# Kernel optimization log

Measured on AMD Instinct MI355X. Metric: run time of the kernel, lower is better.

The kernel has to match this reference:

```python
import jax, jax.numpy as jnp
import numpy as np

N_ATT, N_HEAD, D_K, D_IN = 4, 8, 64, 512
B, T = 128, 512
TEMP = float(np.sqrt(D_K))  # temperature = d_k ** 0.5


def setup_inputs() -> dict:
    key = jax.random.key(0)
    k1, k2, k3 = jax.random.split(key, 3)
    v = jax.random.normal(k1, (B, T, D_IN), jnp.float32)
    # nn.Parameter Q init: normal(0, sqrt(2/d_k))
    Q = jax.random.normal(k2, (N_ATT, N_HEAD, D_K), jnp.float32) * np.sqrt(2.0 / D_K)
    # fc1_k: Linear(d_in, num_attention*n_head*d_k), weight ~ N(0, sqrt(2/d_k))
    Wk = jax.random.normal(k3, (N_ATT * N_HEAD * D_K, D_IN), jnp.float32) * np.sqrt(2.0 / D_K)
    bk = jnp.zeros((N_ATT * N_HEAD * D_K,), jnp.float32)
    return {"v": v, "Q": Q, "Wk": Wk, "bk": bk}


def reference(v, Q, Wk, bk):
    A, H, dk = Q.shape
    Bsz, Tt, d_in = v.shape
    c = d_in // H  # per-head value channels

    # q = stack(Q, dim=2 over batch).view(-1, d_k)  -> [A*H*B, d_k]
    q = jnp.broadcast_to(Q[:, :, None, :], (A, H, Bsz, dk)).reshape(-1, dk)

    # k = fc1_k(v).view(B,T,A,H,dk).permute(3,0,1,2,4).contiguous().view(-1,T,dk)
    # NOTE: this view is a raw C-order reinterpretation (scrambles t/A axes);
    # transpose + reshape reproduces torch's contiguous().view() exactly.
    k = (v @ Wk.T + bk).reshape(Bsz, Tt, A, H, dk)
    k = jnp.transpose(k, (3, 0, 1, 2, 4)).reshape(-1, Tt, dk)  # [H*B*A, T, dk]

    # v heads: stack(v.split(c, dim=-1)).view(H*B, T, c)
    vh = jnp.transpose(v.reshape(Bsz, Tt, H, c), (2, 0, 1, 3)).reshape(H * Bsz, Tt, c)

    # single-query scaled dot-product attention (dropout in eval mode -> identity)
    attn = jnp.einsum('xd,xtd->xt', q, k) / TEMP  # [A*H*B, T]
    attn = jax.nn.softmax(attn, axis=-1)

    # v[:, None].expand(-1, A, -1, -1).reshape(-1, T, c)
    vexp = jnp.broadcast_to(vh[:, None], (H * Bsz, A, Tt, c)).reshape(-1, Tt, c)
    out = jnp.einsum('xt,xtc->xc', attn, vexp)  # [A*H*B, c]

    output = out.reshape(A, H, Bsz, c)
    attn = attn.reshape(A, H, Bsz, Tt)
    return output, attn
```

## Files before the change

kernel.cpp:

```cpp
#include <hip/hip_runtime.h>
#include <hip/hip_bf16.h>
#include <math.h>

#define DIN 512
#define TT  512
#define BSZ 128

using bf16x8 = __attribute__((ext_vector_type(8))) short;
using f32x4  = __attribute__((ext_vector_type(4))) float;

static __device__ __forceinline__ unsigned short f2bf(float x) {
    __hip_bfloat16 h = __float2bfloat16(x);
    return *reinterpret_cast<unsigned short*>(&h);
}
static __device__ __forceinline__ unsigned int pack2(float a, float b) {
    return (unsigned int)f2bf(a) | ((unsigned int)f2bf(b) << 16);
}


__global__ __launch_bounds__(512) void pk_kernel(const float* __restrict__ Q,
                                                 const float* __restrict__ Wk,
                                                 const float* __restrict__ bk,
                                                 unsigned short* __restrict__ Pgb,
                                                 float* __restrict__ qb) {
    const int bid = blockIdx.x;
    const int bg = bid >> 5;
    const int p  = bid & 31;
    const int h  = p >> 2;
    const int ua = p & 3;
    const int a_q = h >> 1;
    const int h_q = (4 * h + bg) & 7;
    const int ch_base = ua * 512 + h * 64;

    __shared__ float qv[64];
    const int tid = threadIdx.x;
    if (tid < 64) qv[tid] = Q[(a_q * 8 + h_q) * 64 + tid];
    __syncthreads();

    const int s = tid;
    float acc = 0.f;
    #pragma unroll 8
    for (int d = 0; d < 64; ++d)
        acc += qv[d] * Wk[(size_t)(ch_base + d) * DIN + s];
    Pgb[(size_t)(bg * 32 + p) * 512 + s] = f2bf(acc * 0.125f);

    if (tid == 0) {
        float sum = 0.f;
        for (int d = 0; d < 64; ++d) sum += qv[d] * bk[ch_base + d];
        qb[bg * 32 + p] = sum * 0.125f;
    }
}

__global__ __launch_bounds__(256) void score_kernel(const float* __restrict__ v,
                                                    const unsigned short* __restrict__ Pgb,
                                                    const float* __restrict__ qb,
                                                    float* __restrict__ attn) {
    const int bid = blockIdx.x;
    const int b = bid >> 2;
    const int j = bid & 3;
    const int bg = b >> 5;
    const int tid = threadIdx.x;
    const int lane = tid & 63;
    const int w = tid >> 6;

    __shared__ char VtB[128 * 80];
    __shared__ char PtB[32 * 1040];
    __shared__ float red2[4][2][4][2];

    const float* vbase = v + ((size_t)b * TT + j * 128) * DIN;

    {
        const int p  = tid >> 3;
        const int sg = tid & 7;
        const uint4* src = (const uint4*)(Pgb + ((size_t)(bg * 32 + p) * 512)) + sg * 8;
        uint4* dst = (uint4*)(PtB + p * 1040 + sg * 128);
        #pragma unroll
        for (int q = 0; q < 8; ++q) dst[q] = src[q];
    }

    const float qv0 = qb[bg * 32 + (lane & 15)];
    const float qv1 = qb[bg * 32 + 16 + (lane & 15)];

    f32x4 acc[2][2];
    #pragma unroll
    for (int i = 0; i < 2; ++i)
        #pragma unroll
        for (int n = 0; n < 2; ++n)
            #pragma unroll
            for (int r = 0; r < 4; ++r) acc[i][n][r] = 0.f;

    const int srow  = tid >> 1;
    const int shalf = tid & 1;
    const float* vsrc = vbase + (size_t)srow * DIN + shalf * 16;
    char* vdst = VtB + srow * 80 + shalf * 32;

    const int akb = (lane >> 4) * 16;
    const char* aptr = VtB + (w * 32 + (lane & 15)) * 80 + akb;
    const char* bptr0 = PtB + ((lane & 15)) * 1040 + akb;
    const char* bptr1 = PtB + (16 + (lane & 15)) * 1040 + akb;

    float4 vrA[4], vrB[4];
    #pragma unroll
    for (int q = 0; q < 4; ++q) vrA[q] = *(const float4*)(vsrc + q * 4);
    #pragma unroll
    for (int q = 0; q < 4; ++q) vrB[q] = *(const float4*)(vsrc + 32 + q * 4);

#define SCORE_STEP(VR, KT)                                                    \
    {                                                                         \
        uint4 lo, hi;                                                         \
        lo.x = pack2(VR[0].x, VR[0].y); lo.y = pack2(VR[0].z, VR[0].w);       \
        lo.z = pack2(VR[1].x, VR[1].y); lo.w = pack2(VR[1].z, VR[1].w);       \
        hi.x = pack2(VR[2].x, VR[2].y); hi.y = pack2(VR[2].z, VR[2].w);       \
        hi.z = pack2(VR[3].x, VR[3].y); hi.w = pack2(VR[3].z, VR[3].w);       \
        *(uint4*)(vdst)      = lo;                                            \
        *(uint4*)(vdst + 16) = hi;                                            \
        __syncthreads();                                                      \
        if ((KT) < 14) {                                                      \
            const float* vn = vsrc + ((KT) + 2) * 32;                         \
            VR[0] = *(const float4*)(vn);                                     \
            VR[1] = *(const float4*)(vn + 4);                                 \
            VR[2] = *(const float4*)(vn + 8);                                 \
            VR[3] = *(const float4*)(vn + 12);                                \
        }                                                                     \
        const int ksb = (KT) * 64;                                            \
        bf16x8 a0 = *(const bf16x8*)(aptr);                                   \
        bf16x8 a1 = *(const bf16x8*)(aptr + 16 * 80);                         \
        bf16x8 b0 = *(const bf16x8*)(bptr0 + ksb);                            \
        bf16x8 b1 = *(const bf16x8*)(bptr1 + ksb);                            \
        acc[0][0] = __builtin_amdgcn_mfma_f32_16x16x32_bf16(a0, b0, acc[0][0], 0, 0, 0); \
        acc[0][1] = __builtin_amdgcn_mfma_f32_16x16x32_bf16(a0, b1, acc[0][1], 0, 0, 0); \
        acc[1][0] = __builtin_amdgcn_mfma_f32_16x16x32_bf16(a1, b0, acc[1][0], 0, 0, 0); \
        acc[1][1] = __builtin_amdgcn_mfma_f32_16x16x32_bf16(a1, b1, acc[1][1], 0, 0, 0); \
        __syncthreads();                                                      \
    }

    for (int kt = 0; kt < 16; kt += 2) {
        SCORE_STEP(vrA, kt);
        SCORE_STEP(vrB, kt + 1);
    }
#undef SCORE_STEP

    float lg[2][8];
    #pragma unroll
    for (int i = 0; i < 2; ++i)
        #pragma unroll
        for (int r = 0; r < 4; ++r) {
            lg[0][i * 4 + r] = acc[i][0][r] + qv0;
            lg[1][i * 4 + r] = acc[i][1][r] + qv1;
        }

    const int hsub = (lane >> 2) & 3;
    float mw[2], sw[2], ev[2][8];
    #pragma unroll
    for (int nt = 0; nt < 2; ++nt) {
        float m = lg[nt][0];
        #pragma unroll
        for (int q = 1; q < 8; ++q) m = fmaxf(m, lg[nt][q]);
        m = fmaxf(m, __shfl_xor(m, 1));
        m = fmaxf(m, __shfl_xor(m, 2));
        m = fmaxf(m, __shfl_xor(m, 16));
        m = fmaxf(m, __shfl_xor(m, 32));
        float s = 0.f;
        #pragma unroll
        for (int q = 0; q < 8; ++q) { ev[nt][q] = __expf(lg[nt][q] - m); s += ev[nt][q]; }
        s += __shfl_xor(s, 1);
        s += __shfl_xor(s, 2);
        s += __shfl_xor(s, 16);
        s += __shfl_xor(s, 32);
        mw[nt] = m; sw[nt] = s;
    }
    if ((lane & 0x33) == 0) {
        #pragma unroll
        for (int nt = 0; nt < 2; ++nt) {
            red2[w][nt][hsub][0] = mw[nt];
            red2[w][nt][hsub][1] = sw[nt];
        }
    }
    __syncthreads();

    #pragma unroll
    for (int nt = 0; nt < 2; ++nt) {
        float M = red2[0][nt][hsub][0];
        M = fmaxf(M, red2[1][nt][hsub][0]);
        M = fmaxf(M, red2[2][nt][hsub][0]);
        M = fmaxf(M, red2[3][nt][hsub][0]);
        float S = 0.f;
        #pragma unroll
        for (int w2 = 0; w2 < 4; ++w2)
            S += __expf(red2[w2][nt][hsub][0] - M) * red2[w2][nt][hsub][1];
        const float factor = __expf(mw[nt] - M) / S;

        const int h = nt * 4 + hsub;
        float* arow = attn + ((size_t)(h * 512 + b * 4 + j)) * 512;
        const int ua = lane & 3;
        #pragma unroll
        for (int i = 0; i < 2; ++i)
            #pragma unroll
            for (int r = 0; r < 4; ++r) {
                const int trow = w * 32 + i * 16 + ((lane >> 4) & 3) * 4 + r;
                arow[trow * 4 + ua] = ev[nt][i * 4 + r] * factor;
            }
    }
}

__global__ __launch_bounds__(256) void pv_kernel(const float* __restrict__ v,
                                                 const float* __restrict__ attn,
                                                 float* __restrict__ out) {
    const int bid = blockIdx.x;
    const int b = bid >> 3;
    const int h = bid & 7;
    const int tid = threadIdx.x;

    __shared__ __align__(16) char smem[34816];
    float (*at)[512]   = reinterpret_cast<float (*)[512]>(smem);
    float (*red)[4][68] = reinterpret_cast<float (*)[4][68]>(smem);

    {
        const int j  = tid >> 6;
        const int u8 = (tid & 63) * 8;
        const float* src = attn + ((size_t)(h * 512 + b * 4 + j)) * 512 + u8;
        *(float4*)&at[j][u8]     = *(const float4*)(src);
        *(float4*)&at[j][u8 + 4] = *(const float4*)(src + 4);
    }
    __syncthreads();

    const int cg = tid & 7;
    const int up = tid >> 3;
    const int c8 = cg * 8;
    const float* vb = v + (size_t)b * TT * DIN + h * 64 + c8;

    float acc[4][8];
    #pragma unroll
    for (int jj = 0; jj < 4; ++jj)
        #pragma unroll
        for (int ci = 0; ci < 8; ++ci) acc[jj][ci] = 0.f;

    float4 rA0 = *(const float4*)(vb + (size_t)up * DIN);
    float4 rA1 = *(const float4*)(vb + (size_t)up * DIN + 4);
    float4 rB0 = *(const float4*)(vb + (size_t)(up + 32) * DIN);
    float4 rB1 = *(const float4*)(vb + (size_t)(up + 32) * DIN + 4);

#define PV_STEP(R0, R1, IT)                                                   \
    {                                                                         \
        const int u = (IT) * 32 + up;                                         \
        const float4 c0 = R0;                                                 \
        const float4 c1 = R1;                                                 \
        if ((IT) < 14) {                                                      \
            const float* pn = vb + (size_t)(u + 64) * DIN;                    \
            R0 = *(const float4*)(pn);                                        \
            R1 = *(const float4*)(pn + 4);                                    \
        }                                                                     \
        const float a0 = at[0][u];                                            \
        const float a1 = at[1][u];                                            \
        const float a2 = at[2][u];                                            \
        const float a3 = at[3][u];                                            \
        acc[0][0] += a0 * c0.x; acc[0][1] += a0 * c0.y; acc[0][2] += a0 * c0.z; acc[0][3] += a0 * c0.w; \
        acc[0][4] += a0 * c1.x; acc[0][5] += a0 * c1.y; acc[0][6] += a0 * c1.z; acc[0][7] += a0 * c1.w; \
        acc[1][0] += a1 * c0.x; acc[1][1] += a1 * c0.y; acc[1][2] += a1 * c0.z; acc[1][3] += a1 * c0.w; \
        acc[1][4] += a1 * c1.x; acc[1][5] += a1 * c1.y; acc[1][6] += a1 * c1.z; acc[1][7] += a1 * c1.w; \
        acc[2][0] += a2 * c0.x; acc[2][1] += a2 * c0.y; acc[2][2] += a2 * c0.z; acc[2][3] += a2 * c0.w; \
        acc[2][4] += a2 * c1.x; acc[2][5] += a2 * c1.y; acc[2][6] += a2 * c1.z; acc[2][7] += a2 * c1.w; \
        acc[3][0] += a3 * c0.x; acc[3][1] += a3 * c0.y; acc[3][2] += a3 * c0.z; acc[3][3] += a3 * c0.w; \
        acc[3][4] += a3 * c1.x; acc[3][5] += a3 * c1.y; acc[3][6] += a3 * c1.z; acc[3][7] += a3 * c1.w; \
    }

    for (int it = 0; it < 16; it += 2) {
        PV_STEP(rA0, rA1, it);
        PV_STEP(rB0, rB1, it + 1);
    }
#undef PV_STEP

    __syncthreads();

    #pragma unroll
    for (int jj = 0; jj < 4; ++jj) {
        float4 w0, w1;
        w0.x = acc[jj][0]; w0.y = acc[jj][1]; w0.z = acc[jj][2]; w0.w = acc[jj][3];
        w1.x = acc[jj][4]; w1.y = acc[jj][5]; w1.z = acc[jj][6]; w1.w = acc[jj][7];
        *(float4*)&red[up][jj][c8]     = w0;
        *(float4*)&red[up][jj][c8 + 4] = w1;
    }
    __syncthreads();

    const int jo = tid >> 6;
    const int c  = tid & 63;
    float s = 0.f;
    #pragma unroll
    for (int r2 = 0; r2 < 32; ++r2) s += red[r2][jo][c];
    out[((size_t)(h * 512 + b * 4 + jo)) * 64 + c] = s;
}

extern "C" void kernel_launch(void* const* d_in, const int* in_sizes, int n_in,
                              void* d_out, int out_size, void* d_ws, size_t ws_size,
                              hipStream_t stream) {
    const float* v  = (const float*)d_in[0];
    const float* Q  = (const float*)d_in[1];
    const float* Wk = (const float*)d_in[2];
    const float* bk = (const float*)d_in[3];

    float* out  = (float*)d_out;
    float* attn = out + 4096 * 64;

    unsigned short* Pgb = (unsigned short*)d_ws;
    float* qb = (float*)(Pgb + 4 * 32 * 512);

    pk_kernel<<<128, 512, 0, stream>>>(Q, Wk, bk, Pgb, qb);
    score_kernel<<<512, 256, 0, stream>>>(v, Pgb, qb, attn);
    pv_kernel<<<1024, 256, 0, stream>>>(v, attn, out);
}
```

Measured before the change: 57.89 us.

## Fuse score/softmax and PV into one per-batch kernel with bf16 attn in LDS

Merges the score and PV kernels into one 1024-thread block per batch element. Attention probabilities are staged in LDS as bf16, so the PV step no longer reads attn back from global memory, and the P tile is streamed per k-step instead of fully preloaded. This removes a kernel launch and the attn round-trip. In exchange the grid shrinks to only 128 blocks (fewer than the CU count), v is read twice within the block, and PV now uses bf16-rounded weights, which lowers precision.

```diff
diff --git a/kernel.cpp b/kernel.cpp
--- a/kernel.cpp
+++ b/kernel.cpp
@@ -4,7 +4,6 @@
 
 #define DIN 512
 #define TT  512
-#define BSZ 128
 
 using bf16x8 = __attribute__((ext_vector_type(8))) short;
 using f32x4  = __attribute__((ext_vector_type(4))) float;
@@ -15,6 +14,9 @@
 }
 static __device__ __forceinline__ unsigned int pack2(float a, float b) {
     return (unsigned int)f2bf(a) | ((unsigned int)f2bf(b) << 16);
+}
+static __device__ __forceinline__ float bf2f(unsigned short u) {
+    return __uint_as_float(((unsigned int)u) << 16);
 }
 
 
@@ -51,32 +53,40 @@
     }
 }
 
-__global__ __launch_bounds__(256) void score_kernel(const float* __restrict__ v,
-                                                    const unsigned short* __restrict__ Pgb,
-                                                    const float* __restrict__ qb,
-                                                    float* __restrict__ attn) {
-    const int bid = blockIdx.x;
-    const int b = bid >> 2;
-    const int j = bid & 3;
-    const int bg = b >> 5;
+__global__ __launch_bounds__(1024, 4) void fused_kernel(
+        const float* __restrict__ v,
+        const unsigned short* __restrict__ Pgb,
+        const float* __restrict__ qb,
+        float* __restrict__ attn,
+        float* __restrict__ out)
+{
+    const int b   = blockIdx.x;
+    const int bg  = b >> 5;
     const int tid = threadIdx.x;
     const int lane = tid & 63;
-    const int w = tid >> 6;
-
-    __shared__ char VtB[128 * 80];
-    __shared__ char PtB[32 * 1040];
-    __shared__ float red2[4][2][4][2];
-
-    const float* vbase = v + ((size_t)b * TT + j * 128) * DIN;
-
-    {
-        const int p  = tid >> 3;
-        const int sg = tid & 7;
-        const uint4* src = (const uint4*)(Pgb + ((size_t)(bg * 32 + p) * 512)) + sg * 8;
-        uint4* dst = (uint4*)(PtB + p * 1040 + sg * 128);
-        #pragma unroll
-        for (int q = 0; q < 8; ++q) dst[q] = src[q];
-    }
+    const int w   = tid >> 6;
+
+    __shared__ __align__(16) char regA[512 * 80];
+    __shared__ __align__(16) char regB[32 * 80];
+    __shared__ float red2[16][2][4][2];
+
+    unsigned short* at16 = (unsigned short*)regA;
+
+    const int srow  = tid >> 1;
+    const int shalf = tid & 1;
+    const float* vsrc = v + ((size_t)b * TT + srow) * DIN + shalf * 16;
+    char* vdst = regA + srow * 80 + shalf * 32;
+
+    const bool pact = (tid < 128);
+    const int  pp   = tid >> 2;
+    const int  pk4  = tid & 3;
+    const unsigned short* psrc = Pgb + ((size_t)(bg * 32 + (pp & 31))) * 512 + pk4 * 8;
+    char* pdst = regB + (pp & 31) * 80 + pk4 * 16;
+
+    const int akb = (lane >> 4) * 16;
+    const char* aptr  = regA + (w * 32 + (lane & 15)) * 80 + akb;
+    const char* bptr0 = regB + (lane & 15) * 80 + akb;
+    const char* bptr1 = regB + (16 + (lane & 15)) * 80 + akb;
 
     const float qv0 = qb[bg * 32 + (lane & 15)];
     const float qv1 = qb[bg * 32 + 16 + (lane & 15)];
@@ -89,23 +99,18 @@
             #pragma unroll
             for (int r = 0; r < 4; ++r) acc[i][n][r] = 0.f;
 
-    const int srow  = tid >> 1;
-    const int shalf = tid & 1;
-    const float* vsrc = vbase + (size_t)srow * DIN + shalf * 16;
-    char* vdst = VtB + srow * 80 + shalf * 32;
-
-    const int akb = (lane >> 4) * 16;
-    const char* aptr = VtB + (w * 32 + (lane & 15)) * 80 + akb;
-    const char* bptr0 = PtB + ((lane & 15)) * 1040 + akb;
-    const char* bptr1 = PtB + (16 + (lane & 15)) * 1040 + akb;
-
     float4 vrA[4], vrB[4];
+    uint4 prA = {0,0,0,0}, prB = {0,0,0,0};
     #pragma unroll
     for (int q = 0; q < 4; ++q) vrA[q] = *(const float4*)(vsrc + q * 4);
     #pragma unroll
     for (int q = 0; q < 4; ++q) vrB[q] = *(const float4*)(vsrc + 32 + q * 4);
-
-#define SCORE_STEP(VR, KT)                                                    \
+    if (pact) {
+        prA = *(const uint4*)(psrc);
+        prB = *(const uint4*)(psrc + 32);
+    }
+
+#define STEP(VR, PR, KT)                                                      \
     {                                                                         \
         uint4 lo, hi;                                                         \
         lo.x = pack2(VR[0].x, VR[0].y); lo.y = pack2(VR[0].z, VR[0].w);       \
@@ -114,6 +119,7 @@
         hi.z = pack2(VR[3].x, VR[3].y); hi.w = pack2(VR[3].z, VR[3].w);       \
         *(uint4*)(vdst)      = lo;                                            \
         *(uint4*)(vdst + 16) = hi;                                            \
+        if (pact) *(uint4*)(pdst) = PR;                                       \
         __syncthreads();                                                      \
         if ((KT) < 14) {                                                      \
             const float* vn = vsrc + ((KT) + 2) * 32;                         \
@@ -121,12 +127,12 @@
             VR[1] = *(const float4*)(vn + 4);                                 \
             VR[2] = *(const float4*)(vn + 8);                                 \
             VR[3] = *(const float4*)(vn + 12);                                \
+            if (pact) PR = *(const uint4*)(psrc + ((KT) + 2) * 32);           \
         }                                                                     \
-        const int ksb = (KT) * 64;                                            \
         bf16x8 a0 = *(const bf16x8*)(aptr);                                   \
         bf16x8 a1 = *(const bf16x8*)(aptr + 16 * 80);                         \
-        bf16x8 b0 = *(const bf16x8*)(bptr0 + ksb);                            \
-        bf16x8 b1 = *(const bf16x8*)(bptr1 + ksb);                            \
+        bf16x8 b0 = *(const bf16x8*)(bptr0);                                  \
+        bf16x8 b1 = *(const bf16x8*)(bptr1);                                  \
         acc[0][0] = __builtin_amdgcn_mfma_f32_16x16x32_bf16(a0, b0, acc[0][0], 0, 0, 0); \
         acc[0][1] = __builtin_amdgcn_mfma_f32_16x16x32_bf16(a0, b1, acc[0][1], 0, 0, 0); \
         acc[1][0] = __builtin_amdgcn_mfma_f32_16x16x32_bf16(a1, b0, acc[1][0], 0, 0, 0); \
@@ -135,10 +141,10 @@
     }
 
     for (int kt = 0; kt < 16; kt += 2) {
-        SCORE_STEP(vrA, kt);
-        SCORE_STEP(vrB, kt + 1);
-    }
-#undef SCORE_STEP
+        STEP(vrA, prA, kt)
+        STEP(vrB, prB, kt + 1)
+    }
+#undef STEP
 
     float lg[2][8];
     #pragma unroll
@@ -150,6 +156,7 @@
         }
 
     const int hsub = (lane >> 2) & 3;
+    const int ua   = lane & 3;
     float mw[2], sw[2], ev[2][8];
     #pragma unroll
     for (int nt = 0; nt < 2; ++nt) {
@@ -178,116 +185,98 @@
     }
     __syncthreads();
 
+    const int jq = w >> 2;
     #pragma unroll
     for (int nt = 0; nt < 2; ++nt) {
-        float M = red2[0][nt][hsub][0];
-        M = fmaxf(M, red2[1][nt][hsub][0]);
-        M = fmaxf(M, red2[2][nt][hsub][0]);
-        M = fmaxf(M, red2[3][nt][hsub][0]);
+        float M = red2[jq * 4 + 0][nt][hsub][0];
+        M = fmaxf(M, red2[jq * 4 + 1][nt][hsub][0]);
+        M = fmaxf(M, red2[jq * 4 + 2][nt][hsub][0]);
+        M = fmaxf(M, red2[jq * 4 + 3][nt][hsub][0]);
         float S = 0.f;
         #pragma unroll
-        for (int w2 = 0; w2 < 4; ++w2)
-            S += __expf(red2[w2][nt][hsub][0] - M) * red2[w2][nt][hsub][1];
+        for (int wg = 0; wg < 4; ++wg)
+            S += __expf(red2[jq * 4 + wg][nt][hsub][0] - M) * red2[jq * 4 + wg][nt][hsub][1];
         const float factor = __expf(mw[nt] - M) / S;
 
         const int h = nt * 4 + hsub;
-        float* arow = attn + ((size_t)(h * 512 + b * 4 + j)) * 512;
-        const int ua = lane & 3;
+        float* arow = attn + ((size_t)(h * 512 + b * 4 + jq)) * 512;
+        unsigned short* atr = at16 + (h * 4 + jq) * 528;
         #pragma unroll
         for (int i = 0; i < 2; ++i)
             #pragma unroll
             for (int r = 0; r < 4; ++r) {
-                const int trow = w * 32 + i * 16 + ((lane >> 4) & 3) * 4 + r;
-                arow[trow * 4 + ua] = ev[nt][i * 4 + r] * factor;
+                const int trow = (w & 3) * 32 + i * 16 + ((lane >> 4) & 3) * 4 + r;
+                const float val = ev[nt][i * 4 + r] * factor;
+                arow[trow * 4 + ua] = val;
+                atr[trow * 4 + ua]  = f2bf(val);
             }
     }
-}
-
-__global__ __launch_bounds__(256) void pv_kernel(const float* __restrict__ v,
-                                                 const float* __restrict__ attn,
-                                                 float* __restrict__ out) {
-    const int bid = blockIdx.x;
-    const int b = bid >> 3;
-    const int h = bid & 7;
-    const int tid = threadIdx.x;
-
-    __shared__ __align__(16) char smem[34816];
-    float (*at)[512]   = reinterpret_cast<float (*)[512]>(smem);
-    float (*red)[4][68] = reinterpret_cast<float (*)[4][68]>(smem);
-
-    {
-        const int j  = tid >> 6;
-        const int u8 = (tid & 63) * 8;
-        const float* src = attn + ((size_t)(h * 512 + b * 4 + j)) * 512 + u8;
-        *(float4*)&at[j][u8]     = *(const float4*)(src);
-        *(float4*)&at[j][u8 + 4] = *(const float4*)(src + 4);
-    }
     __syncthreads();
 
-    const int cg = tid & 7;
-    const int up = tid >> 3;
-    const int c8 = cg * 8;
-    const float* vb = v + (size_t)b * TT * DIN + h * 64 + c8;
-
-    float acc[4][8];
+    const int h3 = tid >> 7;
+    const int c8 = (tid >> 4) & 7;
+    const int up = tid & 15;
+    const float* vb3 = v + (size_t)b * TT * DIN + h3 * 64 + c8 * 8;
+
+    float a3[4][8];
     #pragma unroll
     for (int jj = 0; jj < 4; ++jj)
         #pragma unroll
-        for (int ci = 0; ci < 8; ++ci) acc[jj][ci] = 0.f;
-
-    float4 rA0 = *(const float4*)(vb + (size_t)up * DIN);
-    float4 rA1 = *(const float4*)(vb + (size_t)up * DIN + 4);
-    float4 rB0 = *(const float4*)(vb + (size_t)(up + 32) * DIN);
-    float4 rB1 = *(const float4*)(vb + (size_t)(up + 32) * DIN + 4);
-
-#define PV_STEP(R0, R1, IT)                                                   \
+        for (int ci = 0; ci < 8; ++ci) a3[jj][ci] = 0.f;
+
+    float4 pA0 = *(const float4*)(vb3 + (size_t)up * DIN);
+    float4 pA1 = *(const float4*)(vb3 + (size_t)up * DIN + 4);
+    float4 pB0 = *(const float4*)(vb3 + (size_t)(up + 16) * DIN);
+    float4 pB1 = *(const float4*)(vb3 + (size_t)(up + 16) * DIN + 4);
+
+#define PV3(R0, R1, IT)                                                       \
     {                                                                         \
-        const int u = (IT) * 32 + up;                                         \
-        const float4 c0 = R0;                                                 \
-        const float4 c1 = R1;                                                 \
-        if ((IT) < 14) {                                                      \
-            const float* pn = vb + (size_t)(u + 64) * DIN;                    \
+        const int u = (IT) * 16 + up;                                         \
+        const float4 c0 = R0, c1 = R1;                                        \
+        if ((IT) < 30) {                                                      \
+            const float* pn = vb3 + (size_t)(u + 32) * DIN;                   \
             R0 = *(const float4*)(pn);                                        \
             R1 = *(const float4*)(pn + 4);                                    \
         }                                                                     \
-        const float a0 = at[0][u];                                            \
-        const float a1 = at[1][u];                                            \
-        const float a2 = at[2][u];                                            \
-        const float a3 = at[3][u];                                            \
-        acc[0][0] += a0 * c0.x; acc[0][1] += a0 * c0.y; acc[0][2] += a0 * c0.z; acc[0][3] += a0 * c0.w; \
-        acc[0][4] += a0 * c1.x; acc[0][5] += a0 * c1.y; acc[0][6] += a0 * c1.z; acc[0][7] += a0 * c1.w; \
-        acc[1][0] += a1 * c0.x; acc[1][1] += a1 * c0.y; acc[1][2] += a1 * c0.z; acc[1][3] += a1 * c0.w; \
-        acc[1][4] += a1 * c1.x; acc[1][5] += a1 * c1.y; acc[1][6] += a1 * c1.z; acc[1][7] += a1 * c1.w; \
-        acc[2][0] += a2 * c0.x; acc[2][1] += a2 * c0.y; acc[2][2] += a2 * c0.z; acc[2][3] += a2 * c0.w; \
-        acc[2][4] += a2 * c1.x; acc[2][5] += a2 * c1.y; acc[2][6] += a2 * c1.z; acc[2][7] += a2 * c1.w; \
-        acc[3][0] += a3 * c0.x; acc[3][1] += a3 * c0.y; acc[3][2] += a3 * c0.z; acc[3][3] += a3 * c0.w; \
-        acc[3][4] += a3 * c1.x; acc[3][5] += a3 * c1.y; acc[3][6] += a3 * c1.z; acc[3][7] += a3 * c1.w; \
-    }
-
-    for (int it = 0; it < 16; it += 2) {
-        PV_STEP(rA0, rA1, it);
-        PV_STEP(rB0, rB1, it + 1);
-    }
-#undef PV_STEP
-
-    __syncthreads();
-
-    #pragma unroll
-    for (int jj = 0; jj < 4; ++jj) {
-        float4 w0, w1;
-        w0.x = acc[jj][0]; w0.y = acc[jj][1]; w0.z = acc[jj][2]; w0.w = acc[jj][3];
-        w1.x = acc[jj][4]; w1.y = acc[jj][5]; w1.z = acc[jj][6]; w1.w = acc[jj][7];
-        *(float4*)&red[up][jj][c8]     = w0;
-        *(float4*)&red[up][jj][c8 + 4] = w1;
-    }
-    __syncthreads();
-
-    const int jo = tid >> 6;
-    const int c  = tid & 63;
-    float s = 0.f;
-    #pragma unroll
-    for (int r2 = 0; r2 < 32; ++r2) s += red[r2][jo][c];
-    out[((size_t)(h * 512 + b * 4 + jo)) * 64 + c] = s;
+        const float w0 = bf2f(at16[(h3 * 4 + 0) * 528 + u]);                  \
+        const float w1 = bf2f(at16[(h3 * 4 + 1) * 528 + u]);                  \
+        const float w2 = bf2f(at16[(h3 * 4 + 2) * 528 + u]);                  \
+        const float w3 = bf2f(at16[(h3 * 4 + 3) * 528 + u]);                  \
+        a3[0][0] += w0 * c0.x; a3[0][1] += w0 * c0.y; a3[0][2] += w0 * c0.z; a3[0][3] += w0 * c0.w; \
+        a3[0][4] += w0 * c1.x; a3[0][5] += w0 * c1.y; a3[0][6] += w0 * c1.z; a3[0][7] += w0 * c1.w; \
+        a3[1][0] += w1 * c0.x; a3[1][1] += w1 * c0.y; a3[1][2] += w1 * c0.z; a3[1][3] += w1 * c0.w; \
+        a3[1][4] += w1 * c1.x; a3[1][5] += w1 * c1.y; a3[1][6] += w1 * c1.z; a3[1][7] += w1 * c1.w; \
+        a3[2][0] += w2 * c0.x; a3[2][1] += w2 * c0.y; a3[2][2] += w2 * c0.z; a3[2][3] += w2 * c0.w; \
+        a3[2][4] += w2 * c1.x; a3[2][5] += w2 * c1.y; a3[2][6] += w2 * c1.z; a3[2][7] += w2 * c1.w; \
+        a3[3][0] += w3 * c0.x; a3[3][1] += w3 * c0.y; a3[3][2] += w3 * c0.z; a3[3][3] += w3 * c0.w; \
+        a3[3][4] += w3 * c1.x; a3[3][5] += w3 * c1.y; a3[3][6] += w3 * c1.z; a3[3][7] += w3 * c1.w; \
+    }
+
+    for (int it = 0; it < 32; it += 2) {
+        PV3(pA0, pA1, it)
+        PV3(pB0, pB1, it + 1)
+    }
+#undef PV3
+
+    #pragma unroll
+    for (int off = 1; off <= 8; off <<= 1)
+        #pragma unroll
+        for (int jj = 0; jj < 4; ++jj)
+            #pragma unroll
+            for (int ci = 0; ci < 8; ++ci)
+                a3[jj][ci] += __shfl_xor(a3[jj][ci], off);
+
+    if (up == 0) {
+        #pragma unroll
+        for (int jj = 0; jj < 4; ++jj) {
+            float4 o0, o1;
+            o0.x = a3[jj][0]; o0.y = a3[jj][1]; o0.z = a3[jj][2]; o0.w = a3[jj][3];
+            o1.x = a3[jj][4]; o1.y = a3[jj][5]; o1.z = a3[jj][6]; o1.w = a3[jj][7];
+            float* po = out + ((size_t)(h3 * 512 + b * 4 + jj)) * 64 + c8 * 8;
+            *(float4*)(po)     = o0;
+            *(float4*)(po + 4) = o1;
+        }
+    }
 }
 
 extern "C" void kernel_launch(void* const* d_in, const int* in_sizes, int n_in,
@@ -305,6 +294,5 @@
     float* qb = (float*)(Pgb + 4 * 32 * 512);
 
     pk_kernel<<<128, 512, 0, stream>>>(Q, Wk, bk, Pgb, qb);
-    score_kernel<<<512, 256, 0, stream>>>(v, Pgb, qb, attn);
-    pv_kernel<<<1024, 256, 0, stream>>>(v, attn, out);
-}
+    fused_kernel<<<128, 1024, 0, stream>>>(v, Pgb, qb, attn, out);
+}
```

Measured after the change: 69.87 us. 20.7% more time.

## Merge score and PV kernels into staggered combined launches overlapping batch chunks

Applied to the files above, without the earlier changes.

Replaces the separate score and PV kernels with one combined kernel that dispatches on block index, then launches it five times over 32-batch chunks. Each launch runs score work for the next chunk alongside PV work for the previous chunk, so the two phases overlap and reused v rows may still be in cache. The cost is more kernel launches and a shared-memory footprint sized for the larger branch, which may reduce occupancy for PV blocks.

```diff
diff --git a/kernel.cpp b/kernel.cpp
--- a/kernel.cpp
+++ b/kernel.cpp
@@ -4,7 +4,6 @@
 
 #define DIN 512
 #define TT  512
-#define BSZ 128
 
 using bf16x8 = __attribute__((ext_vector_type(8))) short;
 using f32x4  = __attribute__((ext_vector_type(4))) float;
@@ -51,59 +50,66 @@
     }
 }
 
-__global__ __launch_bounds__(256) void score_kernel(const float* __restrict__ v,
-                                                    const unsigned short* __restrict__ Pgb,
-                                                    const float* __restrict__ qb,
-                                                    float* __restrict__ attn) {
-    const int bid = blockIdx.x;
-    const int b = bid >> 2;
-    const int j = bid & 3;
-    const int bg = b >> 5;
-    const int tid = threadIdx.x;
-    const int lane = tid & 63;
-    const int w = tid >> 6;
-
-    __shared__ char VtB[128 * 80];
-    __shared__ char PtB[32 * 1040];
-    __shared__ float red2[4][2][4][2];
-
-    const float* vbase = v + ((size_t)b * TT + j * 128) * DIN;
-
-    {
-        const int p  = tid >> 3;
-        const int sg = tid & 7;
-        const uint4* src = (const uint4*)(Pgb + ((size_t)(bg * 32 + p) * 512)) + sg * 8;
-        uint4* dst = (uint4*)(PtB + p * 1040 + sg * 128);
-        #pragma unroll
-        for (int q = 0; q < 8; ++q) dst[q] = src[q];
-    }
-
-    const float qv0 = qb[bg * 32 + (lane & 15)];
-    const float qv1 = qb[bg * 32 + 16 + (lane & 15)];
-
-    f32x4 acc[2][2];
-    #pragma unroll
-    for (int i = 0; i < 2; ++i)
-        #pragma unroll
-        for (int n = 0; n < 2; ++n)
-            #pragma unroll
-            for (int r = 0; r < 4; ++r) acc[i][n][r] = 0.f;
-
-    const int srow  = tid >> 1;
-    const int shalf = tid & 1;
-    const float* vsrc = vbase + (size_t)srow * DIN + shalf * 16;
-    char* vdst = VtB + srow * 80 + shalf * 32;
-
-    const int akb = (lane >> 4) * 16;
-    const char* aptr = VtB + (w * 32 + (lane & 15)) * 80 + akb;
-    const char* bptr0 = PtB + ((lane & 15)) * 1040 + akb;
-    const char* bptr1 = PtB + (16 + (lane & 15)) * 1040 + akb;
-
-    float4 vrA[4], vrB[4];
-    #pragma unroll
-    for (int q = 0; q < 4; ++q) vrA[q] = *(const float4*)(vsrc + q * 4);
-    #pragma unroll
-    for (int q = 0; q < 4; ++q) vrB[q] = *(const float4*)(vsrc + 32 + q * 4);
+__global__ __launch_bounds__(256) void combined_kernel(
+        const float* __restrict__ v,
+        const unsigned short* __restrict__ Pgb,
+        const float* __restrict__ qb,
+        float* __restrict__ attn,
+        float* __restrict__ out,
+        int sc_b0, int n_sc, int pv_b0)
+{
+    __shared__ __align__(16) char smem[43776];
+    const int tid  = threadIdx.x;
+
+    if ((int)blockIdx.x < n_sc) {
+        const int item = blockIdx.x;
+        const int b = sc_b0 + (item >> 2);
+        const int j = item & 3;
+        const int bg = b >> 5;
+        const int lane = tid & 63;
+        const int w = tid >> 6;
+
+        char* VtB = smem;
+        char* PtB = smem + 10240;
+        float (*red2)[2][4][2] = reinterpret_cast<float (*)[2][4][2]>(smem + 43520);
+
+        const float* vbase = v + ((size_t)b * TT + j * 128) * DIN;
+
+        {
+            const int p  = tid >> 3;
+            const int sg = tid & 7;
+            const uint4* src = (const uint4*)(Pgb + ((size_t)(bg * 32 + p) * 512)) + sg * 8;
+            uint4* dst = (uint4*)(PtB + p * 1040 + sg * 128);
+            #pragma unroll
+            for (int q = 0; q < 8; ++q) dst[q] = src[q];
+        }
+
+        const float qv0 = qb[bg * 32 + (lane & 15)];
+        const float qv1 = qb[bg * 32 + 16 + (lane & 15)];
+
+        f32x4 acc[2][2];
+        #pragma unroll
+        for (int i = 0; i < 2; ++i)
+            #pragma unroll
+            for (int n = 0; n < 2; ++n)
+                #pragma unroll
+                for (int r = 0; r < 4; ++r) acc[i][n][r] = 0.f;
+
+        const int srow  = tid >> 1;
+        const int shalf = tid & 1;
+        const float* vsrc = vbase + (size_t)srow * DIN + shalf * 16;
+        char* vdst = VtB + srow * 80 + shalf * 32;
+
+        const int akb = (lane >> 4) * 16;
+        const char* aptr  = VtB + (w * 32 + (lane & 15)) * 80 + akb;
+        const char* bptr0 = PtB + ((lane & 15)) * 1040 + akb;
+        const char* bptr1 = PtB + (16 + (lane & 15)) * 1040 + akb;
+
+        float4 vrA[4], vrB[4];
+        #pragma unroll
+        for (int q = 0; q < 4; ++q) vrA[q] = *(const float4*)(vsrc + q * 4);
+        #pragma unroll
+        for (int q = 0; q < 4; ++q) vrB[q] = *(const float4*)(vsrc + 32 + q * 4);
 
 #define SCORE_STEP(VR, KT)                                                    \
     {                                                                         \
@@ -134,111 +140,106 @@
         __syncthreads();                                                      \
     }
 
-    for (int kt = 0; kt < 16; kt += 2) {
-        SCORE_STEP(vrA, kt);
-        SCORE_STEP(vrB, kt + 1);
-    }
+        for (int kt = 0; kt < 16; kt += 2) {
+            SCORE_STEP(vrA, kt);
+            SCORE_STEP(vrB, kt + 1);
+        }
 #undef SCORE_STEP
 
-    float lg[2][8];
-    #pragma unroll
-    for (int i = 0; i < 2; ++i)
-        #pragma unroll
-        for (int r = 0; r < 4; ++r) {
-            lg[0][i * 4 + r] = acc[i][0][r] + qv0;
-            lg[1][i * 4 + r] = acc[i][1][r] + qv1;
-        }
-
-    const int hsub = (lane >> 2) & 3;
-    float mw[2], sw[2], ev[2][8];
-    #pragma unroll
-    for (int nt = 0; nt < 2; ++nt) {
-        float m = lg[nt][0];
-        #pragma unroll
-        for (int q = 1; q < 8; ++q) m = fmaxf(m, lg[nt][q]);
-        m = fmaxf(m, __shfl_xor(m, 1));
-        m = fmaxf(m, __shfl_xor(m, 2));
-        m = fmaxf(m, __shfl_xor(m, 16));
-        m = fmaxf(m, __shfl_xor(m, 32));
-        float s = 0.f;
-        #pragma unroll
-        for (int q = 0; q < 8; ++q) { ev[nt][q] = __expf(lg[nt][q] - m); s += ev[nt][q]; }
-        s += __shfl_xor(s, 1);
-        s += __shfl_xor(s, 2);
-        s += __shfl_xor(s, 16);
-        s += __shfl_xor(s, 32);
-        mw[nt] = m; sw[nt] = s;
-    }
-    if ((lane & 0x33) == 0) {
+        float lg[2][8];
+        #pragma unroll
+        for (int i = 0; i < 2; ++i)
+            #pragma unroll
+            for (int r = 0; r < 4; ++r) {
+                lg[0][i * 4 + r] = acc[i][0][r] + qv0;
+                lg[1][i * 4 + r] = acc[i][1][r] + qv1;
+            }
+
+        const int hsub = (lane >> 2) & 3;
+        float mw[2], sw[2], ev[2][8];
         #pragma unroll
         for (int nt = 0; nt < 2; ++nt) {
-            red2[w][nt][hsub][0] = mw[nt];
-            red2[w][nt][hsub][1] = sw[nt];
-        }
-    }
-    __syncthreads();
-
-    #pragma unroll
-    for (int nt = 0; nt < 2; ++nt) {
-        float M = red2[0][nt][hsub][0];
-        M = fmaxf(M, red2[1][nt][hsub][0]);
-        M = fmaxf(M, red2[2][nt][hsub][0]);
-        M = fmaxf(M, red2[3][nt][hsub][0]);
-        float S = 0.f;
-        #pragma unroll
-        for (int w2 = 0; w2 < 4; ++w2)
-            S += __expf(red2[w2][nt][hsub][0] - M) * red2[w2][nt][hsub][1];
-        const float factor = __expf(mw[nt] - M) / S;
-
-        const int h = nt * 4 + hsub;
-        float* arow = attn + ((size_t)(h * 512 + b * 4 + j)) * 512;
-        const int ua = lane & 3;
-        #pragma unroll
-        for (int i = 0; i < 2; ++i)
-            #pragma unroll
-            for (int r = 0; r < 4; ++r) {
-                const int trow = w * 32 + i * 16 + ((lane >> 4) & 3) * 4 + r;
-                arow[trow * 4 + ua] = ev[nt][i * 4 + r] * factor;
+            float m = lg[nt][0];
+            #pragma unroll
+            for (int q = 1; q < 8; ++q) m = fmaxf(m, lg[nt][q]);
+            m = fmaxf(m, __shfl_xor(m, 1));
+            m = fmaxf(m, __shfl_xor(m, 2));
+            m = fmaxf(m, __shfl_xor(m, 16));
+            m = fmaxf(m, __shfl_xor(m, 32));
+            float s = 0.f;
+            #pragma unroll
+            for (int q = 0; q < 8; ++q) { ev[nt][q] = __expf(lg[nt][q] - m); s += ev[nt][q]; }
+            s += __shfl_xor(s, 1);
+            s += __shfl_xor(s, 2);
+            s += __shfl_xor(s, 16);
+            s += __shfl_xor(s, 32);
+            mw[nt] = m; sw[nt] = s;
+        }
+        if ((lane & 0x33) == 0) {
+            #pragma unroll
+            for (int nt = 0; nt < 2; ++nt) {
+                red2[w][nt][hsub][0] = mw[nt];
+                red2[w][nt][hsub][1] = sw[nt];
             }
-    }
-}
-
-__global__ __launch_bounds__(256) void pv_kernel(const float* __restrict__ v,
-                                                 const float* __restrict__ attn,
-                                                 float* __restrict__ out) {
-    const int bid = blockIdx.x;
-    const int b = bid >> 3;
-    const int h = bid & 7;
-    const int tid = threadIdx.x;
-
-    __shared__ __align__(16) char smem[34816];
-    float (*at)[512]   = reinterpret_cast<float (*)[512]>(smem);
-    float (*red)[4][68] = reinterpret_cast<float (*)[4][68]>(smem);
-
-    {
-        const int j  = tid >> 6;
-        const int u8 = (tid & 63) * 8;
-        const float* src = attn + ((size_t)(h * 512 + b * 4 + j)) * 512 + u8;
-        *(float4*)&at[j][u8]     = *(const float4*)(src);
-        *(float4*)&at[j][u8 + 4] = *(const float4*)(src + 4);
-    }
-    __syncthreads();
-
-    const int cg = tid & 7;
-    const int up = tid >> 3;
-    const int c8 = cg * 8;
-    const float* vb = v + (size_t)b * TT * DIN + h * 64 + c8;
-
-    float acc[4][8];
-    #pragma unroll
-    for (int jj = 0; jj < 4; ++jj)
-        #pragma unroll
-        for (int ci = 0; ci < 8; ++ci) acc[jj][ci] = 0.f;
-
-    float4 rA0 = *(const float4*)(vb + (size_t)up * DIN);
-    float4 rA1 = *(const float4*)(vb + (size_t)up * DIN + 4);
-    float4 rB0 = *(const float4*)(vb + (size_t)(up + 32) * DIN);
-    float4 rB1 = *(const float4*)(vb + (size_t)(up + 32) * DIN + 4);
+        }
+        __syncthreads();
+
+        #pragma unroll
+        for (int nt = 0; nt < 2; ++nt) {
+            float M = red2[0][nt][hsub][0];
+            M = fmaxf(M, red2[1][nt][hsub][0]);
+            M = fmaxf(M, red2[2][nt][hsub][0]);
+            M = fmaxf(M, red2[3][nt][hsub][0]);
+            float S = 0.f;
+            #pragma unroll
+            for (int w2 = 0; w2 < 4; ++w2)
+                S += __expf(red2[w2][nt][hsub][0] - M) * red2[w2][nt][hsub][1];
+            const float factor = __expf(mw[nt] - M) / S;
+
+            const int h = nt * 4 + hsub;
+            float* arow = attn + ((size_t)(h * 512 + b * 4 + j)) * 512;
+            const int ua = lane & 3;
+            #pragma unroll
+            for (int i = 0; i < 2; ++i)
+                #pragma unroll
+                for (int r = 0; r < 4; ++r) {
+                    const int trow = w * 32 + i * 16 + ((lane >> 4) & 3) * 4 + r;
+                    arow[trow * 4 + ua] = ev[nt][i * 4 + r] * factor;
+                }
+        }
+
+    } else {
+        const int item = blockIdx.x - n_sc;
+        const int b = pv_b0 + (item >> 3);
+        const int h = item & 7;
+
+        float (*at)[512]    = reinterpret_cast<float (*)[512]>(smem);
+        float (*red)[4][68] = reinterpret_cast<float (*)[4][68]>(smem);
+
+        {
+            const int jj = tid >> 6;
+            const int u8 = (tid & 63) * 8;
+            const float* src = attn + ((size_t)(h * 512 + b * 4 + jj)) * 512 + u8;
+            *(float4*)&at[jj][u8]     = *(const float4*)(src);
+            *(float4*)&at[jj][u8 + 4] = *(const float4*)(src + 4);
+        }
+        __syncthreads();
+
+        const int cg = tid & 7;
+        const int up = tid >> 3;
+        const int c8 = cg * 8;
+        const float* vb = v + (size_t)b * TT * DIN + h * 64 + c8;
+
+        float acc[4][8];
+        #pragma unroll
+        for (int jj = 0; jj < 4; ++jj)
+            #pragma unroll
+            for (int ci = 0; ci < 8; ++ci) acc[jj][ci] = 0.f;
+
+        float4 rA0 = *(const float4*)(vb + (size_t)up * DIN);
+        float4 rA1 = *(const float4*)(vb + (size_t)up * DIN + 4);
+        float4 rB0 = *(const float4*)(vb + (size_t)(up + 32) * DIN);
+        float4 rB1 = *(const float4*)(vb + (size_t)(up + 32) * DIN + 4);
 
 #define PV_STEP(R0, R1, IT)                                                   \
     {                                                                         \
@@ -264,30 +265,31 @@
         acc[3][4] += a3 * c1.x; acc[3][5] += a3 * c1.y; acc[3][6] += a3 * c1.z; acc[3][7] += a3 * c1.w; \
     }
 
-    for (int it = 0; it < 16; it += 2) {
-        PV_STEP(rA0, rA1, it);
-        PV_STEP(rB0, rB1, it + 1);
+        for (int it = 0; it < 16; it += 2) {
+            PV_STEP(rA0, rA1, it);
+            PV_STEP(rB0, rB1, it + 1);
+        }
+#undef PV_STEP
+
+        __syncthreads();
+
+        #pragma unroll
+        for (int jj = 0; jj < 4; ++jj) {
+            float4 w0, w1;
+            w0.x = acc[jj][0]; w0.y = acc[jj][1]; w0.z = acc[jj][2]; w0.w = acc[jj][3];
+            w1.x = acc[jj][4]; w1.y = acc[jj][5]; w1.z = acc[jj][6]; w1.w = acc[jj][7];
+            *(float4*)&red[up][jj][c8]     = w0;
+            *(float4*)&red[up][jj][c8 + 4] = w1;
+        }
+        __syncthreads();
+
+        const int jo = tid >> 6;
+        const int c  = tid & 63;
+        float s = 0.f;
+        #pragma unroll
+        for (int r2 = 0; r2 < 32; ++r2) s += red[r2][jo][c];
+        out[((size_t)(h * 512 + b * 4 + jo)) * 64 + c] = s;
     }
-#undef PV_STEP
-
-    __syncthreads();
-
-    #pragma unroll
-    for (int jj = 0; jj < 4; ++jj) {
-        float4 w0, w1;
-        w0.x = acc[jj][0]; w0.y = acc[jj][1]; w0.z = acc[jj][2]; w0.w = acc[jj][3];
-        w1.x = acc[jj][4]; w1.y = acc[jj][5]; w1.z = acc[jj][6]; w1.w = acc[jj][7];
-        *(float4*)&red[up][jj][c8]     = w0;
-        *(float4*)&red[up][jj][c8 + 4] = w1;
-    }
-    __syncthreads();
-
-    const int jo = tid >> 6;
-    const int c  = tid & 63;
-    float s = 0.f;
-    #pragma unroll
-    for (int r2 = 0; r2 < 32; ++r2) s += red[r2][jo][c];
-    out[((size_t)(h * 512 + b * 4 + jo)) * 64 + c] = s;
 }
 
 extern "C" void kernel_launch(void* const* d_in, const int* in_sizes, int n_in,
@@ -305,6 +307,10 @@
     float* qb = (float*)(Pgb + 4 * 32 * 512);
 
     pk_kernel<<<128, 512, 0, stream>>>(Q, Wk, bk, Pgb, qb);
-    score_kernel<<<512, 256, 0, stream>>>(v, Pgb, qb, attn);
-    pv_kernel<<<1024, 256, 0, stream>>>(v, attn, out);
-}
+
+    combined_kernel<<<128, 256, 0, stream>>>(v, Pgb, qb, attn, out,  0, 128,  0);
+    combined_kernel<<<384, 256, 0, stream>>>(v, Pgb, qb, attn, out, 32, 128,  0);
+    combined_kernel<<<384, 256, 0, stream>>>(v, Pgb, qb, attn, out, 64, 128, 32);
+    combined_kernel<<<384, 256, 0, stream>>>(v, Pgb, qb, attn, out, 96, 128, 64);
+    combined_kernel<<<256, 256, 0, stream>>>(v, Pgb, qb, attn, out,  0,   0, 96);
+}
```

Result: slower. 70.70 us (+22.1%).

## Fuse score and PV stages with inter-block flag sync and partial reduce

Applied to the files above, without the earlier changes.

Merges the score and PV kernels into one. Each block waits on a per-batch atomic counter until all four T-chunks of its batch have written their attention, then computes a partial PV over its own 128-row slice of v, which is still likely in cache. A small reduce kernel sums the four partials. This removes a second full read of v and one launch, but adds a spin-wait that relies on all 512 blocks being co-resident, and a partial-sum buffer in global memory.

```diff
diff --git a/kernel.cpp b/kernel.cpp
--- a/kernel.cpp
+++ b/kernel.cpp
@@ -4,7 +4,6 @@
 
 #define DIN 512
 #define TT  512
-#define BSZ 128
 
 using bf16x8 = __attribute__((ext_vector_type(8))) short;
 using f32x4  = __attribute__((ext_vector_type(4))) float;
@@ -22,7 +21,8 @@
                                                  const float* __restrict__ Wk,
                                                  const float* __restrict__ bk,
                                                  unsigned short* __restrict__ Pgb,
-                                                 float* __restrict__ qb) {
+                                                 float* __restrict__ qb,
+                                                 int* __restrict__ flags) {
     const int bid = blockIdx.x;
     const int bg = bid >> 5;
     const int p  = bid & 31;
@@ -35,6 +35,7 @@
     __shared__ float qv[64];
     const int tid = threadIdx.x;
     if (tid < 64) qv[tid] = Q[(a_q * 8 + h_q) * 64 + tid];
+    if (tid == 0) flags[bid] = 0;
     __syncthreads();
 
     const int s = tid;
@@ -51,10 +52,12 @@
     }
 }
 
-__global__ __launch_bounds__(256) void score_kernel(const float* __restrict__ v,
+__global__ __launch_bounds__(256) void fused_kernel(const float* __restrict__ v,
                                                     const unsigned short* __restrict__ Pgb,
                                                     const float* __restrict__ qb,
-                                                    float* __restrict__ attn) {
+                                                    float* __restrict__ attn,
+                                                    float* __restrict__ part,
+                                                    int* __restrict__ flags) {
     const int bid = blockIdx.x;
     const int b = bid >> 2;
     const int j = bid & 3;
@@ -63,9 +66,10 @@
     const int lane = tid & 63;
     const int w = tid >> 6;
 
-    __shared__ char VtB[128 * 80];
-    __shared__ char PtB[32 * 1040];
-    __shared__ float red2[4][2][4][2];
+    __shared__ __align__(16) char smem[43776];
+    char* VtB = smem;
+    char* PtB = smem + 10240;
+    float (*red2)[2][4][2] = reinterpret_cast<float (*)[2][4][2]>(smem + 43520);
 
     const float* vbase = v + ((size_t)b * TT + j * 128) * DIN;
 
@@ -95,7 +99,7 @@
     char* vdst = VtB + srow * 80 + shalf * 32;
 
     const int akb = (lane >> 4) * 16;
-    const char* aptr = VtB + (w * 32 + (lane & 15)) * 80 + akb;
+    const char* aptr  = VtB + (w * 32 + (lane & 15)) * 80 + akb;
     const char* bptr0 = PtB + ((lane & 15)) * 1040 + akb;
     const char* bptr1 = PtB + (16 + (lane & 15)) * 1040 + akb;
 
@@ -201,93 +205,80 @@
                 arow[trow * 4 + ua] = ev[nt][i * 4 + r] * factor;
             }
     }
-}
-
-__global__ __launch_bounds__(256) void pv_kernel(const float* __restrict__ v,
-                                                 const float* __restrict__ attn,
-                                                 float* __restrict__ out) {
-    const int bid = blockIdx.x;
-    const int b = bid >> 3;
-    const int h = bid & 7;
-    const int tid = threadIdx.x;
-
-    __shared__ __align__(16) char smem[34816];
-    float (*at)[512]   = reinterpret_cast<float (*)[512]>(smem);
-    float (*red)[4][68] = reinterpret_cast<float (*)[4][68]>(smem);
-
+
+    __syncthreads();
+    if (tid == 0) {
+        __hip_atomic_fetch_add(flags + b, 1, __ATOMIC_RELEASE, __HIP_MEMORY_SCOPE_AGENT);
+        while (__hip_atomic_load(flags + b, __ATOMIC_ACQUIRE, __HIP_MEMORY_SCOPE_AGENT) < 4)
+            __builtin_amdgcn_s_sleep(16);
+    }
+    __syncthreads();
+
+    float (*at32)[132] = reinterpret_cast<float (*)[132]>(smem);
     {
-        const int j  = tid >> 6;
-        const int u8 = (tid & 63) * 8;
-        const float* src = attn + ((size_t)(h * 512 + b * 4 + j)) * 512 + u8;
-        *(float4*)&at[j][u8]     = *(const float4*)(src);
-        *(float4*)&at[j][u8 + 4] = *(const float4*)(src + 4);
-    }
-    __syncthreads();
-
-    const int cg = tid & 7;
-    const int up = tid >> 3;
-    const int c8 = cg * 8;
-    const float* vb = v + (size_t)b * TT * DIN + h * 64 + c8;
-
-    float acc[4][8];
-    #pragma unroll
-    for (int jj = 0; jj < 4; ++jj)
-        #pragma unroll
-        for (int ci = 0; ci < 8; ++ci) acc[jj][ci] = 0.f;
-
-    float4 rA0 = *(const float4*)(vb + (size_t)up * DIN);
-    float4 rA1 = *(const float4*)(vb + (size_t)up * DIN + 4);
-    float4 rB0 = *(const float4*)(vb + (size_t)(up + 32) * DIN);
-    float4 rB1 = *(const float4*)(vb + (size_t)(up + 32) * DIN + 4);
-
-#define PV_STEP(R0, R1, IT)                                                   \
-    {                                                                         \
-        const int u = (IT) * 32 + up;                                         \
-        const float4 c0 = R0;                                                 \
-        const float4 c1 = R1;                                                 \
-        if ((IT) < 14) {                                                      \
-            const float* pn = vb + (size_t)(u + 64) * DIN;                    \
-            R0 = *(const float4*)(pn);                                        \
-            R1 = *(const float4*)(pn + 4);                                    \
-        }                                                                     \
-        const float a0 = at[0][u];                                            \
-        const float a1 = at[1][u];                                            \
-        const float a2 = at[2][u];                                            \
-        const float a3 = at[3][u];                                            \
-        acc[0][0] += a0 * c0.x; acc[0][1] += a0 * c0.y; acc[0][2] += a0 * c0.z; acc[0][3] += a0 * c0.w; \
-        acc[0][4] += a0 * c1.x; acc[0][5] += a0 * c1.y; acc[0][6] += a0 * c1.z; acc[0][7] += a0 * c1.w; \
-        acc[1][0] += a1 * c0.x; acc[1][1] += a1 * c0.y; acc[1][2] += a1 * c0.z; acc[1][3] += a1 * c0.w; \
-        acc[1][4] += a1 * c1.x; acc[1][5] += a1 * c1.y; acc[1][6] += a1 * c1.z; acc[1][7] += a1 * c1.w; \
-        acc[2][0] += a2 * c0.x; acc[2][1] += a2 * c0.y; acc[2][2] += a2 * c0.z; acc[2][3] += a2 * c0.w; \
-        acc[2][4] += a2 * c1.x; acc[2][5] += a2 * c1.y; acc[2][6] += a2 * c1.z; acc[2][7] += a2 * c1.w; \
-        acc[3][0] += a3 * c0.x; acc[3][1] += a3 * c0.y; acc[3][2] += a3 * c0.z; acc[3][3] += a3 * c0.w; \
-        acc[3][4] += a3 * c1.x; acc[3][5] += a3 * c1.y; acc[3][6] += a3 * c1.z; acc[3][7] += a3 * c1.w; \
-    }
-
-    for (int it = 0; it < 16; it += 2) {
-        PV_STEP(rA0, rA1, it);
-        PV_STEP(rB0, rB1, it + 1);
-    }
-#undef PV_STEP
-
-    __syncthreads();
-
-    #pragma unroll
-    for (int jj = 0; jj < 4; ++jj) {
-        float4 w0, w1;
-        w0.x = acc[jj][0]; w0.y = acc[jj][1]; w0.z = acc[jj][2]; w0.w = acc[jj][3];
-        w1.x = acc[jj][4]; w1.y = acc[jj][5]; w1.z = acc[jj][6]; w1.w = acc[jj][7];
-        *(float4*)&red[up][jj][c8]     = w0;
-        *(float4*)&red[up][jj][c8 + 4] = w1;
-    }
-    __syncthreads();
-
-    const int jo = tid >> 6;
-    const int c  = tid & 63;
+        const int rh = tid >> 3;
+        const int g  = tid & 7;
+        const int hh = rh >> 2;
+        const int jp = rh & 3;
+        const float* src = attn + ((size_t)(hh * 512 + b * 4 + jp)) * 512 + j * 128 + g * 16;
+        #pragma unroll
+        for (int q = 0; q < 4; ++q) {
+            float4 t4 = *(const float4*)(src + q * 4);
+            *(float4*)&at32[rh][g * 16 + q * 4] = t4;
+        }
+    }
+    __syncthreads();
+
+    const int hB = tid >> 5;
+    const int cp = tid & 31;
+    const float* vrow = v + ((size_t)b * TT + j * 128) * DIN + hB * 64 + cp * 2;
+    const int h4 = hB * 4;
+
+    float accB[4][2];
+    #pragma unroll
+    for (int jp = 0; jp < 4; ++jp) { accB[jp][0] = 0.f; accB[jp][1] = 0.f; }
+
+    for (int u4 = 0; u4 < 32; ++u4) {
+        const float4 a0 = *(const float4*)&at32[h4 + 0][u4 * 4];
+        const float4 a1 = *(const float4*)&at32[h4 + 1][u4 * 4];
+        const float4 a2 = *(const float4*)&at32[h4 + 2][u4 * 4];
+        const float4 a3 = *(const float4*)&at32[h4 + 3][u4 * 4];
+        const float* pa0 = (const float*)&a0;
+        const float* pa1 = (const float*)&a1;
+        const float* pa2 = (const float*)&a2;
+        const float* pa3 = (const float*)&a3;
+        #pragma unroll
+        for (int s = 0; s < 4; ++s) {
+            const int u = u4 * 4 + s;
+            const float2 vv = *(const float2*)(vrow + (size_t)u * DIN);
+            accB[0][0] += pa0[s] * vv.x; accB[0][1] += pa0[s] * vv.y;
+            accB[1][0] += pa1[s] * vv.x; accB[1][1] += pa1[s] * vv.y;
+            accB[2][0] += pa2[s] * vv.x; accB[2][1] += pa2[s] * vv.y;
+            accB[3][0] += pa3[s] * vv.x; accB[3][1] += pa3[s] * vv.y;
+        }
+    }
+
+    #pragma unroll
+    for (int jp = 0; jp < 4; ++jp) {
+        float2 st; st.x = accB[jp][0]; st.y = accB[jp][1];
+        *(float2*)(part + ((size_t)(b * 4 + j) * 32 + h4 + jp) * 64 + cp * 2) = st;
+    }
+}
+
+__global__ __launch_bounds__(512) void reduce_kernel(const float* __restrict__ part,
+                                                     float* __restrict__ out) {
+    const int e = blockIdx.x * 512 + threadIdx.x;
+    const int x = e >> 6;
+    const int c = e & 63;
+    const int h  = x >> 9;
+    const int b  = (x >> 2) & 127;
+    const int jp = x & 3;
+    const int base = (h * 4 + jp) * 64 + c;
     float s = 0.f;
     #pragma unroll
-    for (int r2 = 0; r2 < 32; ++r2) s += red[r2][jo][c];
-    out[((size_t)(h * 512 + b * 4 + jo)) * 64 + c] = s;
+    for (int j = 0; j < 4; ++j)
+        s += part[(size_t)(b * 4 + j) * 2048 + base];
+    out[e] = s;
 }
 
 extern "C" void kernel_launch(void* const* d_in, const int* in_sizes, int n_in,
@@ -302,9 +293,11 @@
     float* attn = out + 4096 * 64;
 
     unsigned short* Pgb = (unsigned short*)d_ws;
-    float* qb = (float*)(Pgb + 4 * 32 * 512);
-
-    pk_kernel<<<128, 512, 0, stream>>>(Q, Wk, bk, Pgb, qb);
-    score_kernel<<<512, 256, 0, stream>>>(v, Pgb, qb, attn);
-    pv_kernel<<<1024, 256, 0, stream>>>(v, attn, out);
-}
+    float* qb  = (float*)(Pgb + 4 * 32 * 512);
+    int* flags = (int*)(qb + 128);
+    float* part = (float*)(flags + 128);
+
+    pk_kernel<<<128, 512, 0, stream>>>(Q, Wk, bk, Pgb, qb, flags);
+    fused_kernel<<<512, 256, 0, stream>>>(v, Pgb, qb, attn, part, flags);
+    reduce_kernel<<<512, 512, 0, stream>>>(part, out);
+}
```

Result: slower. 87.34 us (+50.9%).
